# Kernel tuning notes

Hardware: AMD Instinct MI355X
Metric: run time of the kernel (lower is better)

## Reference

```python
import jax, jax.numpy as jnp
import numpy as np

B, H, W, C, HID, V, EMB = 16, 24, 96, 1024, 256, 5000, 256
BN_EPS = 1e-5


def _lin(k, fin, fout, s=0.05):
    return jax.random.normal(k, (fin, fout), jnp.float32) * s


def setup_inputs():
    ks = jax.random.split(jax.random.key(0), 24)
    inp = {
        "input_y": jax.random.randint(ks[0], (B,), 0, V),
        "input_hidden": jax.random.normal(ks[1], (B, 1, HID), jnp.float32),
        "img_feature": jax.random.normal(ks[2], (B, C, H, W), jnp.float32),
        "feature_w": W,
        "attention_sum": jnp.zeros((B, 1, H, W), jnp.float32),
        "alpha_t": jax.random.uniform(ks[3], (B, 1, H, W), jnp.float32),
        "feature_h": H,
        "batch_size": B,
        "h_mask": jax.random.randint(ks[4], (B,), 1, H + 1),
        "w_mask": jax.random.randint(ks[5], (B,), 1, W + 1),
        "emb_table": jax.random.normal(ks[6], (V, EMB), jnp.float32) * 0.05,
        "gru1_wi": _lin(ks[7], EMB, 3 * HID), "gru1_wh": _lin(ks[8], HID, 3 * HID),
        "gru1_bi": jnp.zeros((3 * HID,), jnp.float32), "gru1_bh": jnp.zeros((3 * HID,), jnp.float32),
        "fc1_w": _lin(ks[9], HID, 256), "fc1_b": jnp.zeros((256,), jnp.float32),
        "gru2_wi": _lin(ks[10], C, 3 * HID), "gru2_wh": _lin(ks[11], HID, 3 * HID),
        "gru2_bi": jnp.zeros((3 * HID,), jnp.float32), "gru2_bh": jnp.zeros((3 * HID,), jnp.float32),
        "out_w": _lin(ks[12], 128, V), "out_b": jnp.zeros((V,), jnp.float32),
        "emb2_w": _lin(ks[13], 256, 128), "emb2_b": jnp.zeros((128,), jnp.float32),
        "conv1_w": jax.random.normal(ks[14], (1, 1, 3, 3), jnp.float32) * 0.05,
        "conv1_b": jnp.zeros((1,), jnp.float32),
        "conv_tan_w": jax.random.normal(ks[15], (256, 256, 3, 3), jnp.float32) * 0.02,
        "conv_tan_b": jnp.zeros((256,), jnp.float32),
        "fc2_w": _lin(ks[16], HID, 128), "fc2_b": jnp.zeros((128,), jnp.float32),
        "ua_w": _lin(ks[17], C, 256), "ua_b": jnp.zeros((256,), jnp.float32),
        "uf_w": _lin(ks[18], 1, 256), "uf_b": jnp.zeros((256,), jnp.float32),
        "v_w": _lin(ks[19], 256, 1), "v_b": jnp.zeros((1,), jnp.float32),
        "wc_w": _lin(ks[20], C, 128), "wc_b": jnp.zeros((128,), jnp.float32),
        "bn1_gamma": jnp.ones((256,), jnp.float32), "bn1_beta": jnp.zeros((256,), jnp.float32),
        "bn1_mean": jnp.zeros((256,), jnp.float32), "bn1_var": jnp.ones((256,), jnp.float32),
    }
    return inp


def _gru(x, h, wi, wh, bi, bh):
    # PyTorch GRUCell semantics
    gi = x @ wi + bi
    gh = h @ wh + bh
    ir, iz, inn = jnp.split(gi, 3, axis=-1)
    hr, hz, hn = jnp.split(gh, 3, axis=-1)
    r = jax.nn.sigmoid(ir + hr)
    z = jax.nn.sigmoid(iz + hz)
    n = jnp.tanh(inn + r * hn)
    return (1.0 - z) * n + z * h


def _conv(x, w, b):
    y = jax.lax.conv_general_dilated(x, w, (1, 1), 'SAME',
                                     dimension_numbers=('NCHW', 'OIHW', 'NCHW'))
    return y + b[None, :, None, None]


def reference(input_y, input_hidden, img_feature, feature_w, attention_sum, alpha_t,
              feature_h, batch_size, h_mask, w_mask,
              emb_table, gru1_wi, gru1_wh, gru1_bi, gru1_bh, fc1_w, fc1_b,
              gru2_wi, gru2_wh, gru2_bi, gru2_bh, out_w, out_b, emb2_w, emb2_b,
              conv1_w, conv1_b, conv_tan_w, conv_tan_b, fc2_w, fc2_b,
              ua_w, ua_b, uf_w, uf_b, v_w, v_b, wc_w, wc_b,
              bn1_gamma, bn1_beta, bn1_mean, bn1_var):
    b, c, h, w = img_feature.shape
    # per-sample validity mask over the feature map  [B, H, W]
    et_mask = ((jnp.arange(h)[None, :] < h_mask[:, None])[:, :, None]
               & (jnp.arange(w)[None, :] < w_mask[:, None])[:, None, :]).astype(jnp.float32)

    emb = emb_table[input_y]                      # [B, 256] (dropout = identity, eval)
    h0 = input_hidden[:, 0, :]                    # [B, HID]
    st1 = _gru(emb, h0, gru1_wi, gru1_wh, gru1_bi, gru1_bh)
    st1 = st1 @ fc1_w + fc1_b                     # [B, 256]

    alpha_c = _conv(alpha_t, conv1_w, conv1_b)    # [B, 1, H, W]
    att_sum = attention_sum + alpha_c             # coverage accumulator

    img1 = jnp.einsum('bchw,cd->bhwd', img_feature, ua_w) + ua_b  # [B,H,W,256]
    att1 = att_sum[:, 0, :, :, None] * uf_w[0] + uf_b             # Linear(1,256)
    et = st1[:, None, None, :] + img1 + att1      # [B, H, W, 256]

    et_nchw = jnp.transpose(et, (0, 3, 1, 2))
    et_nchw = _conv(et_nchw, conv_tan_w, conv_tan_b)
    et_nchw = et_nchw * et_mask[:, None]
    inv = bn1_gamma / jnp.sqrt(bn1_var + BN_EPS)  # eval-mode BatchNorm2d(256)
    et_nchw = (et_nchw - bn1_mean[None, :, None, None]) * inv[None, :, None, None] \
              + bn1_beta[None, :, None, None]
    et_nchw = jnp.tanh(et_nchw)

    e = jnp.einsum('bchw,c->bhw', et_nchw, v_w[:, 0]) + v_b[0]    # [B, H, W]
    e_exp = jnp.exp(e) * et_mask
    e_sum = jnp.sum(e_exp, axis=(1, 2))
    alpha = e_exp / (e_sum[:, None, None] + 1e-8)                 # masked softmax

    ct = jnp.einsum('bhw,bchw->bc', alpha, img_feature)           # [B, 1024]
    st = _gru(ct, st1, gru2_wi, gru2_wh, gru2_bi, gru2_bh)        # [B, HID]
    hidden_next = st[:, None, :]

    pre = (st @ fc2_w + fc2_b) + (emb @ emb2_w + emb2_b) + (ct @ wc_w + wc_b)  # [B,128]
    output = jax.nn.log_softmax(pre @ out_w + out_b, axis=1)[:, None, :]       # [B,1,V]
    return output, hidden_next, alpha[:, None], att_sum
```

## Files before the change

### kernel.cpp

```cpp
#include <hip/hip_runtime.h>
#include <hip/hip_bf16.h>

#define B   16
#define H   24
#define W   96
#define C   1024
#define HID 256
#define V   5000
#define EMB 256
#define HW  (H*W)
#define BN_EPS 1e-5f
#define H2  (H+2)
#define W2  (W+2)

#define OUT0 0
#define OUT1 (B*V)
#define OUT2 (OUT1 + B*HID)
#define OUT3 (OUT2 + B*HW)

#define WSB_ETP   0
#define WSB_WTB   20873216
#define WSB_UAT   22052864
#define WSB_E     22577152
#define WSB_ST1   22724608
#define WSB_CT    22740992
#define WSB_PRE   22806528
#define WSB_GIGH1 22814720
#define WSB_ST1G  22913024
#define WSB_GH2   22929408
#define WSB_GI2   22986752
#define WSB_STW   23216128

typedef __attribute__((ext_vector_type(8))) short short8;
typedef __attribute__((ext_vector_type(4))) float f32x4;

__device__ inline unsigned short f2bf(float f) {
    union { float f; unsigned int u; } v; v.f = f;
    unsigned int r = v.u + 0x7fffu + ((v.u >> 16) & 1u);
    return (unsigned short)(r >> 16);
}

__global__ __launch_bounds__(256) void k_attsum(
    const float* att_in, const float* alpha_t, const float* cw, const float* cb,
    float* att_out)
{
    int i = blockIdx.x*256 + threadIdx.x;
    int w = i % W; int h = (i / W) % H; int b = i / HW;
    float s = cb[0];
    #pragma unroll
    for (int kh = 0; kh < 3; ++kh) {
        int r = h + kh - 1; if (r < 0 || r >= H) continue;
        #pragma unroll
        for (int kw = 0; kw < 3; ++kw) {
            int c = w + kw - 1; if (c < 0 || c >= W) continue;
            s += alpha_t[(b*H + r)*W + c]*cw[kh*3+kw];
        }
    }
    att_out[i] = att_in[i] + s;
}

__global__ __launch_bounds__(256) void k_wtb(const float* src, unsigned short* dst)
{
    int idx = blockIdx.x*256 + threadIdx.x;
    int c = idx & 255; int o = (idx >> 8) & 255; int khw = idx >> 16;
    dst[(khw*256 + o)*256 + c] = f2bf(src[(o*256 + c)*9 + khw]);
}

__global__ __launch_bounds__(256) void k_uat(const float* src, unsigned short* dst)
{
    int idx = blockIdx.x*256 + threadIdx.x;
    int c = idx & 1023; int d = idx >> 10;
    dst[d*1024 + c] = f2bf(src[c*256 + d]);
}

__global__ __launch_bounds__(256) void k_zero(int4* p)
{
    p[blockIdx.x*256 + threadIdx.x] = make_int4(0,0,0,0);
}

__global__ __launch_bounds__(256) void k_tail1(
    const int* y, const float* emb_table, const float* h0,
    const float* wi, const float* wh, float* gigh)
{
    int virt = blockIdx.x*16;
    int t = threadIdx.x;
    bool gi_mode = virt < 768;
    __shared__ float a_l[16*256];
    for (int i = t; i < 4096; i += 256) {
        int b = i >> 8, k = i & 255;
        a_l[i] = gi_mode ? emb_table[y[b]*EMB + k] : h0[b*HID + k];
    }
    __syncthreads();
    int nl = t & 15, b = t >> 4;
    int n = (gi_mode ? virt : virt - 768) + nl;
    const float* wp = gi_mode ? wi : wh;
    float acc = 0.f;
    #pragma unroll 16
    for (int k = 0; k < 256; ++k) acc += a_l[b*256 + k]*wp[k*768 + n];
    gigh[b*1536 + virt + nl] = acc;
}

__global__ __launch_bounds__(256) void k_comb1(
    const float* gigh, const float* h0, const float* bi, const float* bh, float* st1g)
{
    int b = blockIdx.x, t = threadIdx.x;
    const float* g = gigh + b*1536;
    float ir = g[t] + bi[t], iz = g[256+t] + bi[256+t], in_ = g[512+t] + bi[512+t];
    float hr = g[768+t] + bh[t], hz = g[1024+t] + bh[256+t], hn = g[1280+t] + bh[512+t];
    float r = 1.f/(1.f+__expf(-(ir+hr)));
    float z = 1.f/(1.f+__expf(-(iz+hz)));
    float n = tanhf(in_ + r*hn);
    st1g[b*256+t] = (1.f - z)*n + z*h0[b*HID + t];
}

__global__ __launch_bounds__(256) void k_fc1s(
    const float* st1g, const float* fc1_w, const float* fc1_b, float* st1)
{
    int n0 = blockIdx.x*16, t = threadIdx.x;
    __shared__ float a_l[16*256];
    for (int i = t; i < 4096; i += 256) a_l[i] = st1g[i];
    __syncthreads();
    int nl = t & 15, b = t >> 4;
    float acc = fc1_b[n0+nl];
    #pragma unroll 16
    for (int k = 0; k < 256; ++k) acc += a_l[b*256+k]*fc1_w[k*256 + n0 + nl];
    st1[b*256 + n0 + nl] = acc;
}

__global__ __launch_bounds__(256, 2) void k_et(
    const float* img, const unsigned short* uat, const float* ua_b,
    const float* st1, const float* att_sum, const float* uf_w, const float* uf_b,
    unsigned short* et_p)
{
    int h = blockIdx.x, b = blockIdx.y;
    int t = threadIdx.x;
    int wv = t >> 6, lane = t & 63, q = lane >> 4, ln = lane & 15;
    int n0 = wv*64;
    __shared__ __align__(16) unsigned short a_l[96*72];

    f32x4 acc[24];
    #pragma unroll
    for (int i = 0; i < 24; ++i) acc[i] = (f32x4){0.f,0.f,0.f,0.f};

    for (int c0 = 0; c0 < 1024; c0 += 64) {
        __syncthreads();
        #pragma unroll
        for (int i = t; i < 96*8; i += 256) {
            int c8 = i / 96; int m = i - c8*96;
            const float* sp = img + (size_t)(b*C + c0 + c8*8)*HW + h*W + m;
            union { short8 v; unsigned short u[8]; } pk;
            #pragma unroll
            for (int jj = 0; jj < 8; ++jj) pk.u[jj] = f2bf(sp[jj*HW]);
            *(short8*)&a_l[m*72 + c8*8] = pk.v;
        }
        __syncthreads();
        #pragma unroll
        for (int cs = 0; cs < 64; cs += 32) {
            short8 av[6];
            #pragma unroll
            for (int mf = 0; mf < 6; ++mf)
                av[mf] = *(const short8*)&a_l[(ln + 16*mf)*72 + cs + q*8];
            #pragma unroll
            for (int j = 0; j < 4; ++j) {
                short8 bv = *(const short8*)&uat[(n0 + j*16 + ln)*1024 + c0 + cs + q*8];
                #pragma unroll
                for (int mf = 0; mf < 6; ++mf)
                    acc[mf*4+j] = __builtin_amdgcn_mfma_f32_16x16x32_bf16(av[mf], bv, acc[mf*4+j], 0, 0, 0);
            }
        }
    }

    float att_m[24];
    #pragma unroll
    for (int mf = 0; mf < 6; ++mf)
        #pragma unroll
        for (int r = 0; r < 4; ++r)
            att_m[mf*4+r] = att_sum[(b*H + h)*W + mf*16 + q*4 + r];
    #pragma unroll
    for (int j = 0; j < 4; ++j) {
        int n = n0 + j*16 + ln;
        float s1 = st1[b*256 + n] + ua_b[n];
        float ufw = uf_w[n], ufb = uf_b[n];
        #pragma unroll
        for (int mf = 0; mf < 6; ++mf)
            #pragma unroll
            for (int r = 0; r < 4; ++r) {
                int m = mf*16 + q*4 + r;
                float v = acc[mf*4+j][r] + s1 + att_m[mf*4+r]*ufw + ufb;
                et_p[((size_t)(b*H2 + h + 1)*W2 + (m + 1))*256 + n] = f2bf(v);
            }
    }
}

__global__ __launch_bounds__(256, 2) void k_conv(
    const unsigned short* et_p, const unsigned short* wtb, const float* cb,
    const float* bn_g, const float* bn_b, const float* bn_m, const float* bn_v,
    const float* v_w, const float* v_b, float* e_out)
{
    int h = blockIdx.x, b = blockIdx.y;
    int t = threadIdx.x;
    int wv = t >> 6, lane = t & 63, q = lane >> 4, ln = lane & 15;
    int n0 = wv*64;
    __shared__ __align__(16) unsigned short patch[3*98*72];
    __shared__ float lds_red[4][96];

    f32x4 acc[24];
    #pragma unroll
    for (int i = 0; i < 24; ++i) acc[i] = (f32x4){0.f,0.f,0.f,0.f};

    for (int c0 = 0; c0 < 256; c0 += 64) {
        __syncthreads();
        for (int i = t; i < 2352; i += 256) {
            int kh = i / 784; int r = i - kh*784; int x = r >> 3; int j = r & 7;
            const int4* src = (const int4*)et_p + ((size_t)(b*H2 + h + kh)*W2 + x)*32 + (c0 >> 3) + j;
            ((int4*)patch)[kh*882 + x*9 + j] = *src;
        }
        __syncthreads();
        #pragma unroll
        for (int kh = 0; kh < 3; ++kh) {
            #pragma unroll
            for (int kw = 0; kw < 3; ++kw) {
                const unsigned short* brow = wtb + ((size_t)((kh*3 + kw)*256 + n0 + ln))*256 + c0 + q*8;
                #pragma unroll
                for (int cs = 0; cs < 64; cs += 32) {
                    short8 av[6];
                    #pragma unroll
                    for (int mf = 0; mf < 6; ++mf)
                        av[mf] = *(const short8*)&patch[kh*7056 + (ln + 16*mf + kw)*72 + cs + q*8];
                    #pragma unroll
                    for (int j = 0; j < 4; ++j) {
                        short8 bv = *(const short8*)(brow + j*4096 + cs);
                        #pragma unroll
                        for (int mf = 0; mf < 6; ++mf)
                            acc[mf*4+j] = __builtin_amdgcn_mfma_f32_16x16x32_bf16(av[mf], bv, acc[mf*4+j], 0, 0, 0);
                    }
                }
            }
        }
    }

    float psum[24];
    #pragma unroll
    for (int i = 0; i < 24; ++i) psum[i] = 0.f;
    #pragma unroll
    for (int j = 0; j < 4; ++j) {
        int o = n0 + j*16 + ln;
        float inv  = bn_g[o]*rsqrtf(bn_v[o] + BN_EPS);
        float mean = bn_m[o], beta = bn_b[o], bias = cb[o], vw = v_w[o];
        #pragma unroll
        for (int mf = 0; mf < 6; ++mf)
            #pragma unroll
            for (int r = 0; r < 4; ++r) {
                float x = (acc[mf*4+j][r] + bias - mean)*inv + beta;
                x = fminf(fmaxf(x, -15.f), 15.f);
                float ex = __expf(2.f*x);
                psum[mf*4+r] += ((ex - 1.f)/(ex + 1.f))*vw;
            }
    }
    #pragma unroll
    for (int s = 1; s < 16; s <<= 1)
        #pragma unroll
        for (int i = 0; i < 24; ++i) psum[i] += __shfl_xor(psum[i], s);
    if (ln == 0) {
        #pragma unroll
        for (int mf = 0; mf < 6; ++mf)
            #pragma unroll
            for (int r = 0; r < 4; ++r)
                lds_red[wv][mf*16 + q*4 + r] = psum[mf*4+r];
    }
    __syncthreads();
    if (t < 96)
        e_out[(b*H + h)*W + t] =
            lds_red[0][t] + lds_red[1][t] + lds_red[2][t] + lds_red[3][t] + v_b[0];
}

__global__ __launch_bounds__(256) void k_softmax(
    const float* e, const int* h_mask, const int* w_mask, float* alpha_out)
{
    int b = blockIdx.x, t = threadIdx.x;
    int hm = h_mask[b], wm = w_mask[b];
    __shared__ float red[256];
    float vals[9];
    float loc = 0.f;
    #pragma unroll
    for (int i = 0; i < 9; ++i) {
        int hw = t + i*256;
        int hh = hw / W, ww = hw % W;
        float v = 0.f;
        if (hh < hm && ww < wm) v = __expf(e[b*HW + hw]);
        vals[i] = v; loc += v;
    }
    red[t] = loc; __syncthreads();
    for (int s = 128; s > 0; s >>= 1) { if (t < s) red[t] += red[t+s]; __syncthreads(); }
    float inv = 1.f/(red[0] + 1e-8f);
    #pragma unroll
    for (int i = 0; i < 9; ++i) alpha_out[b*HW + t + i*256] = vals[i]*inv;
}

__global__ __launch_bounds__(256) void k_ct(
    const float* alpha, const float* img, float* ct)
{
    int c = blockIdx.x, b = blockIdx.y, t = threadIdx.x;
    const float* ip = img + (size_t)(b*C + c)*HW;
    const float* ap = alpha + b*HW;
    float s = 0.f;
    for (int i = t; i < HW; i += 256) s += ap[i]*ip[i];
    __shared__ float red[256];
    red[t] = s; __syncthreads();
    for (int st = 128; st > 0; st >>= 1) { if (t < st) red[t] += red[t+st]; __syncthreads(); }
    if (t == 0) ct[b*C + c] = red[0];
}

__global__ __launch_bounds__(256) void k_gh2pe(
    const float* st1, const int* y, const float* emb_table,
    const float* wh, const float* emb2_w, float* gh2)
{
    int virt = blockIdx.x*16, t = threadIdx.x;
    bool ghm = virt < 768;
    __shared__ float a_l[16*256];
    for (int i = t; i < 4096; i += 256) {
        int b = i >> 8, k = i & 255;
        a_l[i] = ghm ? st1[b*256 + k] : emb_table[y[b]*EMB + k];
    }
    __syncthreads();
    int nl = t & 15, b = t >> 4;
    float acc = 0.f;
    if (ghm) {
        int n = virt + nl;
        #pragma unroll 16
        for (int k = 0; k < 256; ++k) acc += a_l[b*256+k]*wh[k*768 + n];
    } else {
        int n = virt - 768 + nl;
        #pragma unroll 16
        for (int k = 0; k < 256; ++k) acc += a_l[b*256+k]*emb2_w[k*128 + n];
    }
    gh2[b*896 + virt + nl] = acc;
}

__global__ __launch_bounds__(256) void k_gi2(
    const float* ct, const float* wi, const float* wc_w, float* gi2p)
{
    int virt = blockIdx.x*16, ks = blockIdx.y, t = threadIdx.x;
    int k0 = ks*256;
    __shared__ float a_l[16*256];
    for (int i = t; i < 4096; i += 256) {
        int b = i >> 8, k = i & 255;
        a_l[i] = ct[b*1024 + k0 + k];
    }
    __syncthreads();
    int nl = t & 15, b = t >> 4;
    float acc = 0.f;
    if (virt < 768) {
        int n = virt + nl;
        #pragma unroll 16
        for (int k = 0; k < 256; ++k) acc += a_l[b*256+k]*wi[(k0+k)*768 + n];
    } else {
        int n = virt - 768 + nl;
        #pragma unroll 16
        for (int k = 0; k < 256; ++k) acc += a_l[b*256+k]*wc_w[(k0+k)*128 + n];
    }
    gi2p[(ks*16 + b)*896 + virt + nl] = acc;
}

__global__ __launch_bounds__(256) void k_comb2(
    const float* gi2p, const float* gh2, const float* st1,
    const float* bi, const float* bh, float* hidden_out, float* st_ws)
{
    int b = blockIdx.x, t = threadIdx.x;
    float ir = bi[t], iz = bi[256+t], in_ = bi[512+t];
    #pragma unroll
    for (int ks = 0; ks < 4; ++ks) {
        const float* g = gi2p + (ks*16 + b)*896;
        ir += g[t]; iz += g[256+t]; in_ += g[512+t];
    }
    const float* gh = gh2 + b*896;
    float hr = gh[t] + bh[t], hz = gh[256+t] + bh[256+t], hn = gh[512+t] + bh[512+t];
    float h = st1[b*256+t];
    float r = 1.f/(1.f+__expf(-(ir+hr)));
    float z = 1.f/(1.f+__expf(-(iz+hz)));
    float n = tanhf(in_ + r*hn);
    float s = (1.f - z)*n + z*h;
    hidden_out[b*HID + t] = s;
    st_ws[b*256 + t] = s;
}

__global__ __launch_bounds__(256) void k_fc2s(
    const float* st_ws, const float* fc2_w, const float* fc2_b,
    const float* gh2, const float* emb2_b, const float* gi2p,
    const float* wc_b, float* pre)
{
    int n0 = blockIdx.x*16, t = threadIdx.x;
    __shared__ float a_l[16*256];
    for (int i = t; i < 4096; i += 256) a_l[i] = st_ws[i];
    __syncthreads();
    int nl = t & 15, b = t >> 4;
    int n = n0 + nl;
    float acc = fc2_b[n] + emb2_b[n] + wc_b[n] + gh2[b*896 + 768 + n];
    #pragma unroll
    for (int ks = 0; ks < 4; ++ks) acc += gi2p[(ks*16 + b)*896 + 768 + n];
    #pragma unroll 16
    for (int k = 0; k < 256; ++k) acc += a_l[b*256+k]*fc2_w[k*128 + n];
    pre[b*128 + n] = acc;
}

__global__ __launch_bounds__(256) void k_logits(
    const float* pre, const float* out_w, const float* out_b, float* out)
{
    int j0 = blockIdx.x*64, t = threadIdx.x;
    __shared__ float pre_l[16*128];
    for (int i = t; i < 2048; i += 256) pre_l[i] = pre[i];
    __syncthreads();
    int jl = t & 63, bg = t >> 6;
    int j = j0 + jl;
    if (j >= V) return;
    float acc0=0.f, acc1=0.f, acc2=0.f, acc3=0.f;
    const float* pl = pre_l + bg*4*128;
    #pragma unroll 8
    for (int k = 0; k < 128; ++k) {
        float wv = out_w[k*V + j];
        acc0 += pl[k]*wv; acc1 += pl[128+k]*wv; acc2 += pl[256+k]*wv; acc3 += pl[384+k]*wv;
    }
    float ob = out_b[j];
    out[(bg*4+0)*V + j] = acc0 + ob;
    out[(bg*4+1)*V + j] = acc1 + ob;
    out[(bg*4+2)*V + j] = acc2 + ob;
    out[(bg*4+3)*V + j] = acc3 + ob;
}

__global__ __launch_bounds__(1024) void k_lsm(float* out)
{
    int b = blockIdx.x, t = threadIdx.x;
    __shared__ float red[1024];
    float lg[5]; float mx = -1e30f;
    #pragma unroll
    for (int i = 0; i < 5; ++i) {
        int j = t + i*1024;
        lg[i] = (j < V) ? out[b*V + j] : -1e30f;
        mx = fmaxf(mx, lg[i]);
    }
    red[t] = mx; __syncthreads();
    for (int s = 512; s > 0; s >>= 1) { if (t < s) red[t] = fmaxf(red[t], red[t+s]); __syncthreads(); }
    float gmax = red[0]; __syncthreads();
    float se = 0.f;
    #pragma unroll
    for (int i = 0; i < 5; ++i) { int j = t + i*1024; if (j < V) se += __expf(lg[i] - gmax); }
    red[t] = se; __syncthreads();
    for (int s = 512; s > 0; s >>= 1) { if (t < s) red[t] += red[t+s]; __syncthreads(); }
    float lse = logf(red[0]);
    #pragma unroll
    for (int i = 0; i < 5; ++i) { int j = t + i*1024; if (j < V) out[b*V + j] = lg[i] - gmax - lse; }
}

extern "C" void kernel_launch(void* const* d_in, const int* in_sizes, int n_in,
                              void* d_out, int out_size, void* d_ws, size_t ws_size,
                              hipStream_t stream)
{
    const int*   input_y      = (const int*)  d_in[0];
    const float* input_hidden = (const float*)d_in[1];
    const float* img          = (const float*)d_in[2];
    const float* attention    = (const float*)d_in[4];
    const float* alpha_t      = (const float*)d_in[5];
    const int*   h_mask       = (const int*)  d_in[8];
    const int*   w_mask       = (const int*)  d_in[9];
    const float* emb_table    = (const float*)d_in[10];
    const float* gru1_wi      = (const float*)d_in[11];
    const float* gru1_wh      = (const float*)d_in[12];
    const float* gru1_bi      = (const float*)d_in[13];
    const float* gru1_bh      = (const float*)d_in[14];
    const float* fc1_w        = (const float*)d_in[15];
    const float* fc1_b        = (const float*)d_in[16];
    const float* gru2_wi      = (const float*)d_in[17];
    const float* gru2_wh      = (const float*)d_in[18];
    const float* gru2_bi      = (const float*)d_in[19];
    const float* gru2_bh      = (const float*)d_in[20];
    const float* out_w        = (const float*)d_in[21];
    const float* out_b        = (const float*)d_in[22];
    const float* emb2_w       = (const float*)d_in[23];
    const float* emb2_b       = (const float*)d_in[24];
    const float* conv1_w      = (const float*)d_in[25];
    const float* conv1_b      = (const float*)d_in[26];
    const float* conv_tan_w   = (const float*)d_in[27];
    const float* conv_tan_b   = (const float*)d_in[28];
    const float* fc2_w        = (const float*)d_in[29];
    const float* fc2_b        = (const float*)d_in[30];
    const float* ua_w         = (const float*)d_in[31];
    const float* ua_b         = (const float*)d_in[32];
    const float* uf_w         = (const float*)d_in[33];
    const float* uf_b         = (const float*)d_in[34];
    const float* v_w          = (const float*)d_in[35];
    const float* v_b          = (const float*)d_in[36];
    const float* wc_w         = (const float*)d_in[37];
    const float* wc_b         = (const float*)d_in[38];
    const float* bn1_gamma    = (const float*)d_in[39];
    const float* bn1_beta     = (const float*)d_in[40];
    const float* bn1_mean     = (const float*)d_in[41];
    const float* bn1_var      = (const float*)d_in[42];

    float* out = (float*)d_out;
    char*  ws  = (char*)d_ws;
    unsigned short* et_p = (unsigned short*)(ws + WSB_ETP);
    unsigned short* wtb  = (unsigned short*)(ws + WSB_WTB);
    unsigned short* uat  = (unsigned short*)(ws + WSB_UAT);
    float* e_buf = (float*)(ws + WSB_E);
    float* st1   = (float*)(ws + WSB_ST1);
    float* ct    = (float*)(ws + WSB_CT);
    float* pre   = (float*)(ws + WSB_PRE);
    float* gigh1 = (float*)(ws + WSB_GIGH1);
    float* st1g  = (float*)(ws + WSB_ST1G);
    float* gh2   = (float*)(ws + WSB_GH2);
    float* gi2p  = (float*)(ws + WSB_GI2);
    float* st_w  = (float*)(ws + WSB_STW);

    float* out_logits = out + OUT0;
    float* out_hidden = out + OUT1;
    float* out_alpha  = out + OUT2;
    float* out_attsum = out + OUT3;

    k_tail1<<<96, 256, 0, stream>>>(input_y, emb_table, input_hidden,
                                    gru1_wi, gru1_wh, gigh1);
    k_comb1<<<B, 256, 0, stream>>>(gigh1, input_hidden, gru1_bi, gru1_bh, st1g);
    k_fc1s<<<16, 256, 0, stream>>>(st1g, fc1_w, fc1_b, st1);
    k_attsum<<<(B*HW)/256, 256, 0, stream>>>(attention, alpha_t, conv1_w, conv1_b, out_attsum);
    k_wtb<<<(9*256*256)/256, 256, 0, stream>>>(conv_tan_w, wtb);
    k_uat<<<(256*1024)/256, 256, 0, stream>>>(ua_w, uat);
    k_zero<<<(B*H2*W2*256/8)/256, 256, 0, stream>>>((int4*)et_p);
    k_et<<<dim3(H, B), 256, 0, stream>>>(img, uat, ua_b, st1, out_attsum,
                                         uf_w, uf_b, et_p);
    k_conv<<<dim3(H, B), 256, 0, stream>>>(et_p, wtb, conv_tan_b,
                                           bn1_gamma, bn1_beta, bn1_mean, bn1_var,
                                           v_w, v_b, e_buf);
    k_softmax<<<B, 256, 0, stream>>>(e_buf, h_mask, w_mask, out_alpha);
    k_ct<<<dim3(C, B), 256, 0, stream>>>(out_alpha, img, ct);
    k_gh2pe<<<56, 256, 0, stream>>>(st1, input_y, emb_table, gru2_wh, emb2_w, gh2);
    k_gi2<<<dim3(56, 4), 256, 0, stream>>>(ct, gru2_wi, wc_w, gi2p);
    k_comb2<<<B, 256, 0, stream>>>(gi2p, gh2, st1, gru2_bi, gru2_bh, out_hidden, st_w);
    k_fc2s<<<8, 256, 0, stream>>>(st_w, fc2_w, fc2_b, gh2, emb2_b, gi2p, wc_b, pre);
    k_logits<<<(V + 63)/64, 256, 0, stream>>>(pre, out_w, out_b, out_logits);
    k_lsm<<<B, 1024, 0, stream>>>(out_logits);
}
```

Baseline: 583.1 us.

## Pre-transpose image to bf16 channel-last, drop LDS staging, split N across blocks

Adds a kernel that converts the image once into a bf16 [B,HW,C] layout. The attention-projection GEMM, the context reduction and the conv GEMM now read their operands straight from global memory instead of staging them in LDS. The et and conv kernels are split into two N-halves per block, which doubles the grid and halves the accumulator registers; conv writes two partial energy maps that the softmax kernel sums. The context vector is now computed with fewer blocks plus atomicAdd, and it reads bf16 image values, which lowers precision. In exchange this costs an extra full-image read and a 75MB write, and removes LDS reuse of the A tiles.

```diff
diff --git a/kernel.cpp b/kernel.cpp
--- a/kernel.cpp
+++ b/kernel.cpp
@@ -18,18 +18,19 @@
 #define OUT2 (OUT1 + B*HID)
 #define OUT3 (OUT2 + B*HW)
 
-#define WSB_ETP   0
-#define WSB_WTB   20873216
-#define WSB_UAT   22052864
-#define WSB_E     22577152
-#define WSB_ST1   22724608
-#define WSB_CT    22740992
-#define WSB_PRE   22806528
-#define WSB_GIGH1 22814720
-#define WSB_ST1G  22913024
-#define WSB_GH2   22929408
-#define WSB_GI2   22986752
-#define WSB_STW   23216128
+#define WSB_IMGT  0
+#define WSB_ETP   75497472
+#define WSB_WTB   96370688
+#define WSB_UAT   97550336
+#define WSB_E     98074624
+#define WSB_ST1   98369536
+#define WSB_CT    98385920
+#define WSB_PRE   98451456
+#define WSB_GIGH1 98459648
+#define WSB_ST1G  98557952
+#define WSB_GH2   98574336
+#define WSB_GI2   98631680
+#define WSB_STW   98861056
 
 typedef __attribute__((ext_vector_type(8))) short short8;
 typedef __attribute__((ext_vector_type(4))) float f32x4;
@@ -38,6 +39,37 @@
     union { float f; unsigned int u; } v; v.f = f;
     unsigned int r = v.u + 0x7fffu + ((v.u >> 16) & 1u);
     return (unsigned short)(r >> 16);
+}
+__device__ inline float bf2f(unsigned short u) {
+    union { unsigned int u; float f; } v; v.u = ((unsigned int)u) << 16;
+    return v.f;
+}
+
+__global__ __launch_bounds__(256) void k_imgT(const float* img, unsigned short* imgT)
+{
+    int hw0 = blockIdx.x*128, c1 = blockIdx.y*128, b = blockIdx.z;
+    int t = threadIdx.x;
+    __shared__ unsigned short tr[128*136];
+    #pragma unroll
+    for (int i = 0; i < 16; ++i) {
+        int flat = i*1024 + t*4;
+        int r = flat >> 7;
+        int col = flat & 127;
+        float4 v = *(const float4*)&img[((size_t)(b*C + c1 + r))*HW + hw0 + col];
+        tr[(col+0)*136 + r] = f2bf(v.x);
+        tr[(col+1)*136 + r] = f2bf(v.y);
+        tr[(col+2)*136 + r] = f2bf(v.z);
+        tr[(col+3)*136 + r] = f2bf(v.w);
+    }
+    __syncthreads();
+    #pragma unroll
+    for (int i = 0; i < 8; ++i) {
+        int flat = i*2048 + t*8;
+        int orow = flat >> 7;
+        int oc = flat & 127;
+        *(short8*)&imgT[((size_t)(b*HW) + hw0 + orow)*1024 + c1 + oc] =
+            *(const short8*)&tr[orow*136 + oc];
+    }
 }
 
 __global__ __launch_bounds__(256) void k_attsum(
@@ -127,46 +159,34 @@
     st1[b*256 + n0 + nl] = acc;
 }
 
-__global__ __launch_bounds__(256, 2) void k_et(
-    const float* img, const unsigned short* uat, const float* ua_b,
+__global__ __launch_bounds__(256) void k_et(
+    const unsigned short* imgT, const unsigned short* uat, const float* ua_b,
     const float* st1, const float* att_sum, const float* uf_w, const float* uf_b,
     unsigned short* et_p)
 {
-    int h = blockIdx.x, b = blockIdx.y;
+    int h = blockIdx.x, ny = blockIdx.y, b = blockIdx.z;
     int t = threadIdx.x;
     int wv = t >> 6, lane = t & 63, q = lane >> 4, ln = lane & 15;
-    int n0 = wv*64;
-    __shared__ __align__(16) unsigned short a_l[96*72];
-
-    f32x4 acc[24];
-    #pragma unroll
-    for (int i = 0; i < 24; ++i) acc[i] = (f32x4){0.f,0.f,0.f,0.f};
-
-    for (int c0 = 0; c0 < 1024; c0 += 64) {
-        __syncthreads();
-        #pragma unroll
-        for (int i = t; i < 96*8; i += 256) {
-            int c8 = i / 96; int m = i - c8*96;
-            const float* sp = img + (size_t)(b*C + c0 + c8*8)*HW + h*W + m;
-            union { short8 v; unsigned short u[8]; } pk;
-            #pragma unroll
-            for (int jj = 0; jj < 8; ++jj) pk.u[jj] = f2bf(sp[jj*HW]);
-            *(short8*)&a_l[m*72 + c8*8] = pk.v;
-        }
-        __syncthreads();
-        #pragma unroll
-        for (int cs = 0; cs < 64; cs += 32) {
-            short8 av[6];
+    int n0 = ny*128 + wv*32;
+
+    f32x4 acc[12];
+    #pragma unroll
+    for (int i = 0; i < 12; ++i) acc[i] = (f32x4){0.f,0.f,0.f,0.f};
+
+    const unsigned short* abase = imgT + ((size_t)(b*HW) + h*W)*1024 + q*8;
+    const unsigned short* bbase = uat + (size_t)(n0 + ln)*1024 + q*8;
+
+    for (int c0 = 0; c0 < 1024; c0 += 32) {
+        short8 av[6];
+        #pragma unroll
+        for (int mf = 0; mf < 6; ++mf)
+            av[mf] = *(const short8*)(abase + (size_t)(ln + 16*mf)*1024 + c0);
+        #pragma unroll
+        for (int j = 0; j < 2; ++j) {
+            short8 bv = *(const short8*)(bbase + (size_t)(j*16)*1024 + c0);
             #pragma unroll
             for (int mf = 0; mf < 6; ++mf)
-                av[mf] = *(const short8*)&a_l[(ln + 16*mf)*72 + cs + q*8];
-            #pragma unroll
-            for (int j = 0; j < 4; ++j) {
-                short8 bv = *(const short8*)&uat[(n0 + j*16 + ln)*1024 + c0 + cs + q*8];
-                #pragma unroll
-                for (int mf = 0; mf < 6; ++mf)
-                    acc[mf*4+j] = __builtin_amdgcn_mfma_f32_16x16x32_bf16(av[mf], bv, acc[mf*4+j], 0, 0, 0);
-            }
+                acc[mf*2+j] = __builtin_amdgcn_mfma_f32_16x16x32_bf16(av[mf], bv, acc[mf*2+j], 0, 0, 0);
         }
     }
 
@@ -177,7 +197,7 @@
         for (int r = 0; r < 4; ++r)
             att_m[mf*4+r] = att_sum[(b*H + h)*W + mf*16 + q*4 + r];
     #pragma unroll
-    for (int j = 0; j < 4; ++j) {
+    for (int j = 0; j < 2; ++j) {
         int n = n0 + j*16 + ln;
         float s1 = st1[b*256 + n] + ua_b[n];
         float ufw = uf_w[n], ufb = uf_b[n];
@@ -186,54 +206,45 @@
             #pragma unroll
             for (int r = 0; r < 4; ++r) {
                 int m = mf*16 + q*4 + r;
-                float v = acc[mf*4+j][r] + s1 + att_m[mf*4+r]*ufw + ufb;
+                float v = acc[mf*2+j][r] + s1 + att_m[mf*4+r]*ufw + ufb;
                 et_p[((size_t)(b*H2 + h + 1)*W2 + (m + 1))*256 + n] = f2bf(v);
             }
     }
 }
 
-__global__ __launch_bounds__(256, 2) void k_conv(
+__global__ __launch_bounds__(256) void k_conv(
     const unsigned short* et_p, const unsigned short* wtb, const float* cb,
     const float* bn_g, const float* bn_b, const float* bn_m, const float* bn_v,
-    const float* v_w, const float* v_b, float* e_out)
-{
-    int h = blockIdx.x, b = blockIdx.y;
+    const float* v_w, float* e_part)
+{
+    int h = blockIdx.x, ny = blockIdx.y, b = blockIdx.z;
     int t = threadIdx.x;
     int wv = t >> 6, lane = t & 63, q = lane >> 4, ln = lane & 15;
-    int n0 = wv*64;
-    __shared__ __align__(16) unsigned short patch[3*98*72];
+    int n0 = ny*128 + wv*32;
     __shared__ float lds_red[4][96];
 
-    f32x4 acc[24];
-    #pragma unroll
-    for (int i = 0; i < 24; ++i) acc[i] = (f32x4){0.f,0.f,0.f,0.f};
-
-    for (int c0 = 0; c0 < 256; c0 += 64) {
-        __syncthreads();
-        for (int i = t; i < 2352; i += 256) {
-            int kh = i / 784; int r = i - kh*784; int x = r >> 3; int j = r & 7;
-            const int4* src = (const int4*)et_p + ((size_t)(b*H2 + h + kh)*W2 + x)*32 + (c0 >> 3) + j;
-            ((int4*)patch)[kh*882 + x*9 + j] = *src;
-        }
-        __syncthreads();
-        #pragma unroll
-        for (int kh = 0; kh < 3; ++kh) {
-            #pragma unroll
-            for (int kw = 0; kw < 3; ++kw) {
-                const unsigned short* brow = wtb + ((size_t)((kh*3 + kw)*256 + n0 + ln))*256 + c0 + q*8;
+    f32x4 acc[12];
+    #pragma unroll
+    for (int i = 0; i < 12; ++i) acc[i] = (f32x4){0.f,0.f,0.f,0.f};
+
+    #pragma unroll
+    for (int kh = 0; kh < 3; ++kh) {
+        #pragma unroll
+        for (int kw = 0; kw < 3; ++kw) {
+            const unsigned short* arow = et_p + ((size_t)(b*H2 + h + kh)*W2 + kw)*256 + q*8;
+            const unsigned short* brow = wtb + ((size_t)((kh*3 + kw)*256 + n0 + ln))*256 + q*8;
+            #pragma unroll 2
+            for (int c0 = 0; c0 < 256; c0 += 32) {
+                short8 av[6];
                 #pragma unroll
-                for (int cs = 0; cs < 64; cs += 32) {
-                    short8 av[6];
+                for (int mf = 0; mf < 6; ++mf)
+                    av[mf] = *(const short8*)(arow + (size_t)(ln + 16*mf)*256 + c0);
+                #pragma unroll
+                for (int j = 0; j < 2; ++j) {
+                    short8 bv = *(const short8*)(brow + (size_t)(j*16)*256 + c0);
                     #pragma unroll
                     for (int mf = 0; mf < 6; ++mf)
-                        av[mf] = *(const short8*)&patch[kh*7056 + (ln + 16*mf + kw)*72 + cs + q*8];
-                    #pragma unroll
-                    for (int j = 0; j < 4; ++j) {
-                        short8 bv = *(const short8*)(brow + j*4096 + cs);
-                        #pragma unroll
-                        for (int mf = 0; mf < 6; ++mf)
-                            acc[mf*4+j] = __builtin_amdgcn_mfma_f32_16x16x32_bf16(av[mf], bv, acc[mf*4+j], 0, 0, 0);
-                    }
+                        acc[mf*2+j] = __builtin_amdgcn_mfma_f32_16x16x32_bf16(av[mf], bv, acc[mf*2+j], 0, 0, 0);
                 }
             }
         }
@@ -243,7 +254,7 @@
     #pragma unroll
     for (int i = 0; i < 24; ++i) psum[i] = 0.f;
     #pragma unroll
-    for (int j = 0; j < 4; ++j) {
+    for (int j = 0; j < 2; ++j) {
         int o = n0 + j*16 + ln;
         float inv  = bn_g[o]*rsqrtf(bn_v[o] + BN_EPS);
         float mean = bn_m[o], beta = bn_b[o], bias = cb[o], vw = v_w[o];
@@ -251,7 +262,7 @@
         for (int mf = 0; mf < 6; ++mf)
             #pragma unroll
             for (int r = 0; r < 4; ++r) {
-                float x = (acc[mf*4+j][r] + bias - mean)*inv + beta;
+                float x = (acc[mf*2+j][r] + bias - mean)*inv + beta;
                 x = fminf(fmaxf(x, -15.f), 15.f);
                 float ex = __expf(2.f*x);
                 psum[mf*4+r] += ((ex - 1.f)/(ex + 1.f))*vw;
@@ -270,15 +281,17 @@
     }
     __syncthreads();
     if (t < 96)
-        e_out[(b*H + h)*W + t] =
-            lds_red[0][t] + lds_red[1][t] + lds_red[2][t] + lds_red[3][t] + v_b[0];
+        e_part[(size_t)ny*(B*HW) + (b*H + h)*W + t] =
+            lds_red[0][t] + lds_red[1][t] + lds_red[2][t] + lds_red[3][t];
 }
 
 __global__ __launch_bounds__(256) void k_softmax(
-    const float* e, const int* h_mask, const int* w_mask, float* alpha_out)
+    const float* e_part, const int* h_mask, const int* w_mask, const float* v_b,
+    float* alpha_out)
 {
     int b = blockIdx.x, t = threadIdx.x;
     int hm = h_mask[b], wm = w_mask[b];
+    float vb = v_b[0];
     __shared__ float red[256];
     float vals[9];
     float loc = 0.f;
@@ -287,7 +300,8 @@
         int hw = t + i*256;
         int hh = hw / W, ww = hw % W;
         float v = 0.f;
-        if (hh < hm && ww < wm) v = __expf(e[b*HW + hw]);
+        if (hh < hm && ww < wm)
+            v = __expf(e_part[b*HW + hw] + e_part[B*HW + b*HW + hw] + vb);
         vals[i] = v; loc += v;
     }
     red[t] = loc; __syncthreads();
@@ -297,18 +311,29 @@
     for (int i = 0; i < 9; ++i) alpha_out[b*HW + t + i*256] = vals[i]*inv;
 }
 
+__global__ __launch_bounds__(256) void k_ct0(float* ct)
+{
+    ct[blockIdx.x*256 + threadIdx.x] = 0.f;
+}
+
 __global__ __launch_bounds__(256) void k_ct(
-    const float* alpha, const float* img, float* ct)
-{
-    int c = blockIdx.x, b = blockIdx.y, t = threadIdx.x;
-    const float* ip = img + (size_t)(b*C + c)*HW;
-    const float* ap = alpha + b*HW;
-    float s = 0.f;
-    for (int i = t; i < HW; i += 256) s += ap[i]*ip[i];
-    __shared__ float red[256];
-    red[t] = s; __syncthreads();
-    for (int st = 128; st > 0; st >>= 1) { if (t < st) red[t] += red[t+st]; __syncthreads(); }
-    if (t == 0) ct[b*C + c] = red[0];
+    const float* alpha, const unsigned short* imgT, float* ct)
+{
+    int s = blockIdx.x, b = blockIdx.y, t = threadIdx.x;
+    int cg = (t & 127)*8, half = t >> 7;
+    float acc[8];
+    #pragma unroll
+    for (int j = 0; j < 8; ++j) acc[j] = 0.f;
+    for (int i = 0; i < 96; ++i) {
+        int hw = s*192 + i*2 + half;
+        float a = alpha[b*HW + hw];
+        union { short8 v; unsigned short u[8]; } pk;
+        pk.v = *(const short8*)&imgT[((size_t)(b*HW) + hw)*1024 + cg];
+        #pragma unroll
+        for (int j = 0; j < 8; ++j) acc[j] += a*bf2f(pk.u[j]);
+    }
+    #pragma unroll
+    for (int j = 0; j < 8; ++j) atomicAdd(&ct[b*1024 + cg + j], acc[j]);
 }
 
 __global__ __launch_bounds__(256) void k_gh2pe(
@@ -498,10 +523,11 @@
 
     float* out = (float*)d_out;
     char*  ws  = (char*)d_ws;
+    unsigned short* imgT = (unsigned short*)(ws + WSB_IMGT);
     unsigned short* et_p = (unsigned short*)(ws + WSB_ETP);
     unsigned short* wtb  = (unsigned short*)(ws + WSB_WTB);
     unsigned short* uat  = (unsigned short*)(ws + WSB_UAT);
-    float* e_buf = (float*)(ws + WSB_E);
+    float* e_part = (float*)(ws + WSB_E);
     float* st1   = (float*)(ws + WSB_ST1);
     float* ct    = (float*)(ws + WSB_CT);
     float* pre   = (float*)(ws + WSB_PRE);
@@ -516,6 +542,7 @@
     float* out_alpha  = out + OUT2;
     float* out_attsum = out + OUT3;
 
+    k_imgT<<<dim3(HW/128, C/128, B), 256, 0, stream>>>(img, imgT);
     k_tail1<<<96, 256, 0, stream>>>(input_y, emb_table, input_hidden,
                                     gru1_wi, gru1_wh, gigh1);
     k_comb1<<<B, 256, 0, stream>>>(gigh1, input_hidden, gru1_bi, gru1_bh, st1g);
@@ -524,13 +551,14 @@
     k_wtb<<<(9*256*256)/256, 256, 0, stream>>>(conv_tan_w, wtb);
     k_uat<<<(256*1024)/256, 256, 0, stream>>>(ua_w, uat);
     k_zero<<<(B*H2*W2*256/8)/256, 256, 0, stream>>>((int4*)et_p);
-    k_et<<<dim3(H, B), 256, 0, stream>>>(img, uat, ua_b, st1, out_attsum,
-                                         uf_w, uf_b, et_p);
-    k_conv<<<dim3(H, B), 256, 0, stream>>>(et_p, wtb, conv_tan_b,
-                                           bn1_gamma, bn1_beta, bn1_mean, bn1_var,
-                                           v_w, v_b, e_buf);
-    k_softmax<<<B, 256, 0, stream>>>(e_buf, h_mask, w_mask, out_alpha);
-    k_ct<<<dim3(C, B), 256, 0, stream>>>(out_alpha, img, ct);
+    k_et<<<dim3(H, 2, B), 256, 0, stream>>>(imgT, uat, ua_b, st1, out_attsum,
+                                            uf_w, uf_b, et_p);
+    k_conv<<<dim3(H, 2, B), 256, 0, stream>>>(et_p, wtb, conv_tan_b,
+                                              bn1_gamma, bn1_beta, bn1_mean, bn1_var,
+                                              v_w, e_part);
+    k_softmax<<<B, 256, 0, stream>>>(e_part, h_mask, w_mask, v_b, out_alpha);
+    k_ct0<<<(B*C)/256, 256, 0, stream>>>(ct);
+    k_ct<<<dim3(12, B), 256, 0, stream>>>(out_alpha, imgT, ct);
     k_gh2pe<<<56, 256, 0, stream>>>(st1, input_y, emb_table, gru2_wh, emb2_w, gh2);
     k_gi2<<<dim3(56, 4), 256, 0, stream>>>(ct, gru2_wi, wc_w, gi2p);
     k_comb2<<<B, 256, 0, stream>>>(gi2p, gh2, st1, gru2_bi, gru2_bh, out_hidden, st_w);
```

New measurement: 737.6 us. +26.5%, slower.
